# Kernel tuning notes

Hardware: AMD Instinct MI355X
Metric: run time of the kernel (lower is better)

Reference implementation:

```python
import jax, jax.numpy as jnp
import numpy as np
from math import sqrt

NUM_ENT = 100000
NUM_REL = 237  # base; rel table has 2*NUM_REL rows
DIM = 200
HALF = DIM // 2


def _lrelu(x, slope):
    return jnp.where(x >= 0, x, slope * x)


def setup_inputs() -> dict:
    key = jax.random.key(0)
    ks = jax.random.split(key, 20)
    s = 0.02
    inp = {
        'edge_index': jax.random.randint(ks[0], (2, 500000), 0, NUM_ENT),
        'edge_type': jax.random.randint(ks[1], (500000,), 0, 2 * NUM_REL),
        'toTest': jax.random.randint(ks[2], (131072, 2), 0, NUM_ENT),
        'ent_emb': s * jax.random.normal(ks[3], (NUM_ENT, DIM), jnp.float32),
        'rel_emb': s * jax.random.normal(ks[4], (2 * NUM_REL, DIM), jnp.float32),
        'W': s * jax.random.normal(ks[5], (DIM, DIM), jnp.float32),
        'W_loop': s * jax.random.normal(ks[6], (DIM, DIM), jnp.float32),
        'W_rel': s * jax.random.normal(ks[7], (DIM, DIM), jnp.float32),
        'trans_w': s * jax.random.normal(ks[8], (DIM, HALF), jnp.float32),
        'trans_b': jnp.zeros((HALF,), jnp.float32),
        'q_w': s * jax.random.normal(ks[9], (HALF, 128), jnp.float32),
        'q_b': jnp.zeros((128,), jnp.float32),
        'k_w': s * jax.random.normal(ks[10], (HALF, 128), jnp.float32),
        'k_b': jnp.zeros((128,), jnp.float32),
        'w1': s * jax.random.normal(ks[11], (DIM * 2 + 1 + 2 * NUM_REL, 2048), jnp.float32),
        'b1': jnp.zeros((2048,), jnp.float32),
        'w2': s * jax.random.normal(ks[12], (2048, 512), jnp.float32),
        'b2': jnp.zeros((512,), jnp.float32),
        'w3': s * jax.random.normal(ks[13], (512, 1), jnp.float32),
        'b3': jnp.zeros((1,), jnp.float32),
    }
    return inp


def reference(ent_emb, rel_emb, W, W_loop, W_rel, trans_w, trans_b,
              q_w, q_b, k_w, k_b, w1, b1, w2, b2, w3, b3,
              edge_index, edge_type, toTest):
    # --- CompGCN base layer ('sub' composition, degree-normalized scatter-add) ---
    src, dst = edge_index[0], edge_index[1]
    msg = (ent_emb[src] - rel_emb[edge_type]) @ W          # [E, D] gather + GEMM
    deg = jax.ops.segment_sum(jnp.ones_like(dst, jnp.float32), dst, num_segments=NUM_ENT)
    norm = jax.lax.rsqrt(jnp.maximum(deg, 1.0))
    agg = jax.ops.segment_sum(msg, dst, num_segments=NUM_ENT) * norm[:, None]
    all_ent = jnp.tanh(agg + ent_emb @ W_loop)             # [num_ent, D]
    all_rel = rel_emb @ W_rel                              # [2*num_rel, D]

    # --- PairRE test scoring path ---
    head_rel = all_rel[:, :HALF]                           # [2R, D/2]
    tail_rel = all_rel[:, HALF:]
    te = all_ent[toTest]                                   # [N, 2, D] gather
    ee = te @ trans_w + trans_b                            # [N, 2, D/2]
    h_e, t_e = ee[:, 0], ee[:, 1]
    atta = ((h_e @ q_w + q_b) * (t_e @ k_w + k_b)).sum(-1, keepdims=True) / sqrt(DIM)
    relSim = h_e @ head_rel.T - t_e @ tail_rel.T           # [N, 2R]
    cat = jnp.concatenate([te[:, 0], te[:, 1], atta, relSim], axis=1)
    h1 = _lrelu(cat @ w1 + b1, 1e-4)
    h2 = _lrelu(h1 @ w2 + b2, 1e-3)
    return jax.nn.sigmoid(h2 @ w3 + b3)                    # [N, 1]
```

## Files before the change

kernel.cpp:

```cpp
#include <hip/hip_runtime.h>

typedef unsigned short u16;
typedef unsigned long long u64;
typedef __attribute__((ext_vector_type(8))) short bf8;
typedef __attribute__((ext_vector_type(4))) float fx4;

#define N_ENT   100000
#define N_EDGE  500000
#define N_TEST  131072
#define EDIM    200
#define AE_LD   224
#define NB_SCAN 391

__device__ __forceinline__ u16 f2bf(float f) {
  union { float f; unsigned u; } c; c.f = f;
  return (u16)((c.u + 0x7FFFu + ((c.u >> 16) & 1u)) >> 16);
}
__device__ __forceinline__ float bf2f(u16 h) {
  union { unsigned u; float f; } c; c.u = ((unsigned)h) << 16;
  return c.f;
}
__device__ __forceinline__ void gload16(const u16* g, u16* l) {
  __builtin_amdgcn_global_load_lds(
      (const __attribute__((address_space(1))) void*)g,
      (__attribute__((address_space(3))) void*)l, 16, 0, 0);
}

#define BK 32
#define EPS 72

template<int TM, int WN>
__global__ __launch_bounds__(64 * 2 * WN) void gemm_t(
    const u16* __restrict__ A, long lda,
    const u16* __restrict__ B, long ldb,
    u16* __restrict__ out, long ldOut,
    int K, int NBN,
    const int* __restrict__ rowIdx, int idxMode, int mClamp,
    int mValid, int nValid, int nStore,
    const float* __restrict__ bias, int act, float slope,
    const u16* __restrict__ qbuf, const float* __restrict__ auxF,
    float* __restrict__ dotOut)
{
  constexpr int BM = TM * 32;
  constexpr int BN = WN * 64;
  constexpr int BUFS = (BM + BN) * BK;
  __shared__ __align__(16) u16 smem[2 * BUFS];
  const int tid  = threadIdx.x;
  const int wave = tid >> 6, lane = tid & 63;
  const int wr = (wave / WN) * (TM * 16), wc = (wave % WN) * 64;
  const int fr = lane & 15, fq = lane >> 4;

  const int nwg = gridDim.x;
  const int orig = blockIdx.x;
  const int q = nwg >> 3, rr = nwg & 7;
  const int xcd = orig & 7, j = orig >> 3;
  const int wgid = (xcd < rr ? xcd * (q + 1) : rr * (q + 1) + (xcd - rr) * q) + j;
  const long bm = (long)(wgid / NBN) * BM;
  const long bn = (long)(wgid % NBN) * BN;

  const int srow = wave * 32;
  const int kc = (((lane & 3) ^ ((lane >> 3) & 3)) * 8);
  long a0[2], a1[2], boff[2];
  #pragma unroll
  for (int h = 0; h < 2; ++h) {
    long gmRow = bm + srow + h * 16 + (lane >> 2);
    long b0, b1;
    if (idxMode == 0) {
      long gm = (gmRow >= mClamp) ? (mClamp - 1) : gmRow;
      b0 = gm * lda; b1 = b0;
    } else if (idxMode == 2) {
      b0 = (long)rowIdx[2 * gmRow] * lda; b1 = b0;
    } else if (idxMode == 3) {
      b0 = (long)rowIdx[2 * gmRow + 1] * lda; b1 = b0;
    } else {
      b0 = (long)rowIdx[2 * gmRow] * lda;
      b1 = (long)rowIdx[2 * gmRow + 1] * lda - 224;
    }
    a0[h] = b0 + kc; a1[h] = b1 + kc;
    boff[h] = (bn + srow + h * 16 + (lane >> 2)) * ldb + kc;
  }

  auto STAGE = [&](int buf, int k0) {
    u16* Ad = smem + buf * BUFS;
    u16* Bd = Ad + BM * BK;
    const bool lo = (k0 + kc) < 224;
    #pragma unroll
    for (int h = 0; h < 2; ++h) {
      const long ao = (idxMode == 4) ? (lo ? a0[h] : a1[h]) : a0[h];
      gload16(A + ao + k0, &Ad[(srow + h * 16) * BK]);
      gload16(B + boff[h] + k0, &Bd[(srow + h * 16) * BK]);
    }
  };

  fx4 zero4 = {0.f, 0.f, 0.f, 0.f};
  fx4 acc[TM][4];
  #pragma unroll
  for (int i = 0; i < TM; ++i)
    #pragma unroll
    for (int j2 = 0; j2 < 4; ++j2) acc[i][j2] = zero4;

  const int NT = K / BK;
  STAGE(0, 0);
  for (int t = 0; t < NT; ++t) {
    const int cur = t & 1;
    if (t + 1 < NT) {
      STAGE(cur ^ 1, (t + 1) * BK);
      __builtin_amdgcn_sched_barrier(0);
      asm volatile("s_waitcnt vmcnt(4)" ::: "memory");
    } else {
      __builtin_amdgcn_sched_barrier(0);
      asm volatile("s_waitcnt vmcnt(0)" ::: "memory");
    }
    __builtin_amdgcn_sched_barrier(0);
    __builtin_amdgcn_s_barrier();
    __builtin_amdgcn_sched_barrier(0);
    {
      const u16* Ac = smem + cur * BUFS;
      const u16* Bc = Ac + BM * BK;
      bf8 aF[TM], bF[4];
      const int rslot = (fq ^ ((fr >> 1) & 3)) * 8;
      #pragma unroll
      for (int mt = 0; mt < TM; ++mt)
        aF[mt] = *(const bf8*)&Ac[(wr + mt * 16 + fr) * BK + rslot];
      #pragma unroll
      for (int nt = 0; nt < 4; ++nt)
        bF[nt] = *(const bf8*)&Bc[(wc + nt * 16 + fr) * BK + rslot];
      #pragma unroll
      for (int mt = 0; mt < TM; ++mt)
        #pragma unroll
        for (int nt = 0; nt < 4; ++nt)
          acc[mt][nt] = __builtin_amdgcn_mfma_f32_16x16x32_bf16(aF[mt], bF[nt], acc[mt][nt], 0, 0, 0);
    }
    __builtin_amdgcn_sched_barrier(0);
    __builtin_amdgcn_s_barrier();
    __builtin_amdgcn_sched_barrier(0);
  }

  if (act == 3 || act == 4) {
    #pragma unroll
    for (int mt = 0; mt < TM; ++mt) {
      #pragma unroll
      for (int r = 0; r < 4; ++r) {
        const long gm = bm + wr + mt * 16 + fq * 4 + r;
        float p = 0.f;
        #pragma unroll
        for (int nt = 0; nt < 4; ++nt) {
          const long gn = bn + wc + nt * 16 + fr;
          float v = acc[mt][nt][r] + bias[gn];
          if (act == 3) p += v * bf2f(qbuf[gm * 128 + gn]);
          else { v = (v >= 0.f) ? v : v * slope; p += v * auxF[gn]; }
        }
        p += __shfl_xor(p, 1, 64); p += __shfl_xor(p, 2, 64);
        p += __shfl_xor(p, 4, 64); p += __shfl_xor(p, 8, 64);
        if (fr == 0 && gm < mValid)
          atomicAdd(&dotOut[gm], (act == 3) ? p * 0.07071067811865475f : p);
      }
    }
    return;
  }

  u16* ep = smem + wave * (32 * EPS);
  #pragma unroll
  for (int p = 0; p < TM / 2; ++p) {
    #pragma unroll
    for (int mt2 = 0; mt2 < 2; ++mt2) {
      const int mt = 2 * p + mt2;
      #pragma unroll
      for (int r = 0; r < 4; ++r) {
        const int lrl = mt2 * 16 + fq * 4 + r;
        const long gm = bm + wr + mt * 16 + fq * 4 + r;
        const float attaV = (act == 5) ? dotOut[gm] : 0.f;
        #pragma unroll
        for (int nt = 0; nt < 4; ++nt) {
          const long gn = bn + wc + nt * 16 + fr;
          float v = 0.f;
          if (gn < nValid) {
            v = acc[mt][nt][r];
            if (bias) v += bias[gn];
            if (act == 1) v = tanhf(v);
            else if (act == 5) { v += attaV * auxF[gn]; v = (v >= 0.f) ? v : v * slope; }
          }
          ep[lrl * EPS + nt * 16 + fr] = f2bf(v);
        }
      }
    }
    #pragma unroll
    for (int it = 0; it < 4; ++it) {
      const int lr = it * 8 + (lane >> 3);
      const int lc = (lane & 7) * 8;
      const long gm = bm + wr + p * 32 + lr;
      const long gn = bn + wc + lc;
      if (gm < mValid && gn + 7 < nStore)
        *(bf8*)(out + gm * ldOut + gn) = *(const bf8*)&ep[lr * EPS + lc];
    }
  }
}

__global__ void hist_kernel(const int* __restrict__ ei, int* __restrict__ cnt) {
  int e = blockIdx.x * 256 + threadIdx.x;
  if (e < N_EDGE) atomicAdd(&cnt[ei[N_EDGE + e]], 1);
}
__global__ void scanA_kernel(const int* __restrict__ cnt, int* __restrict__ offs,
                             int* __restrict__ blockSums) {
  __shared__ int s[256];
  int gid = blockIdx.x * 256 + threadIdx.x;
  int v = (gid < N_ENT) ? cnt[gid] : 0;
  s[threadIdx.x] = v;
  __syncthreads();
  for (int off = 1; off < 256; off <<= 1) {
    int t = (threadIdx.x >= off) ? s[threadIdx.x - off] : 0;
    __syncthreads();
    s[threadIdx.x] += t;
    __syncthreads();
  }
  if (gid < N_ENT) offs[gid] = s[threadIdx.x] - v;
  if (threadIdx.x == 255) blockSums[blockIdx.x] = s[255];
}
__global__ void scanB_kernel(const int* __restrict__ blockSums, int* __restrict__ blockOffs) {
  __shared__ int s[512];
  int v = (threadIdx.x < NB_SCAN) ? blockSums[threadIdx.x] : 0;
  s[threadIdx.x] = v;
  __syncthreads();
  for (int off = 1; off < 512; off <<= 1) {
    int t = (threadIdx.x >= off) ? s[threadIdx.x - off] : 0;
    __syncthreads();
    s[threadIdx.x] += t;
    __syncthreads();
  }
  if (threadIdx.x < NB_SCAN) blockOffs[threadIdx.x] = s[threadIdx.x] - v;
}
__global__ void scanC_kernel(int* __restrict__ offs, const int* __restrict__ blockOffs) {
  int gid = blockIdx.x * 256 + threadIdx.x;
  if (gid < N_ENT) offs[gid] += blockOffs[blockIdx.x];
}
__global__ void place_kernel(const int* __restrict__ ei, const int* __restrict__ et,
                             const int* __restrict__ offs, int* __restrict__ cursor,
                             int* __restrict__ sortedSrc, int* __restrict__ sortedT) {
  int e = blockIdx.x * 256 + threadIdx.x;
  if (e >= N_EDGE) return;
  int dst = ei[N_EDGE + e];
  int pos = offs[dst] + atomicAdd(&cursor[dst], 1);
  sortedSrc[pos] = ei[e];
  sortedT[pos]   = et[e];
}
__global__ void agg_A1_kernel(const int* __restrict__ offs, const int* __restrict__ cnt,
                              const int* __restrict__ sortedSrc, const int* __restrict__ sortedT,
                              const float* __restrict__ ent_emb, const float* __restrict__ rel_emb,
                              u16* __restrict__ A1) {
  const int r = blockIdx.x * 4 + (threadIdx.x >> 6);
  if (r >= N_ENT) return;
  const int lane = threadIdx.x & 63;
  const int beg = offs[r], n = cnt[r];
  u16* row = A1 + (size_t)r * 416;
  if (lane < 50) {
    float4 a = {0.f, 0.f, 0.f, 0.f};
    for (int e = 0; e < n; ++e) {
      const int s = sortedSrc[beg + e], t = sortedT[beg + e];
      float4 x = ((const float4*)(ent_emb + (size_t)s * EDIM))[lane];
      float4 y = ((const float4*)(rel_emb + (size_t)t * EDIM))[lane];
      a.x += x.x - y.x; a.y += x.y - y.y; a.z += x.z - y.z; a.w += x.w - y.w;
    }
    const float nm = rsqrtf(fmaxf((float)n, 1.f));
    u64 p = (u64)f2bf(a.x * nm) | ((u64)f2bf(a.y * nm) << 16)
          | ((u64)f2bf(a.z * nm) << 32) | ((u64)f2bf(a.w * nm) << 48);
    *(u64*)(row + 4 * lane) = p;
    float4 e = ((const float4*)(ent_emb + (size_t)r * EDIM))[lane];
    u64 q = (u64)f2bf(e.x) | ((u64)f2bf(e.y) << 16)
          | ((u64)f2bf(e.z) << 32) | ((u64)f2bf(e.w) << 48);
    *(u64*)(row + 200 + 4 * lane) = q;
  }
  if (lane < 16) row[400 + lane] = 0;
}

__global__ void build_B1T(const float* __restrict__ W, const float* __restrict__ W_loop,
                          u16* __restrict__ B1T)
{
  int idx = blockIdx.x * 256 + threadIdx.x;
  if (idx >= 256 * 416) return;
  int n = idx / 416, k = idx % 416;
  float v = 0.f;
  if (n < 200) {
    if (k < 200) v = W[k * 200 + n];
    else if (k < 400) v = W_loop[(k - 200) * 200 + n];
  }
  B1T[idx] = f2bf(v);
}
__global__ void all_rel_kernel(const float* __restrict__ rel_emb, const float* __restrict__ W_rel,
                               float* __restrict__ all_rel)
{
  int r = blockIdx.x, c = threadIdx.x;
  if (c >= 200) return;
  const float* re = rel_emb + r * 200;
  float a = 0.f;
  for (int k = 0; k < 200; ++k) a += re[k] * W_rel[k * 200 + c];
  all_rel[r * 200 + c] = a;
}
__global__ void pq_kernel(const float* __restrict__ all_rel, const float* __restrict__ w1,
                          float* __restrict__ PQ) {
  int idx = blockIdx.x * 256 + threadIdx.x;
  if (idx >= 2 * 100 * 2048) return;
  int n = idx & 2047, m = (idx >> 11) % 100, sel = idx / 204800;
  float a = 0.f;
  for (int r = 0; r < 474; ++r)
    a += all_rel[r * 200 + sel * 100 + m] * w1[(size_t)(401 + r) * 2048 + n];
  PQ[idx] = a;
}
__global__ void p2_kernel(const float* __restrict__ trans_w, const float* __restrict__ PQ,
                          float* __restrict__ P2) {
  int idx = blockIdx.x * 256 + threadIdx.x;
  if (idx >= 2 * 200 * 2048) return;
  int n = idx & 2047, k = (idx >> 11) % 200, sel = idx / 409600;
  const float* pq = PQ + sel * 204800;
  float a = 0.f;
  for (int m = 0; m < 100; ++m) a += trans_w[k * 100 + m] * pq[m * 2048 + n];
  P2[idx] = a;
}
__global__ void w1eff_kernel(const float* __restrict__ w1, const float* __restrict__ P2,
                             u16* __restrict__ W1eff) {
  int idx = blockIdx.x * 256 + threadIdx.x;
  if (idx >= 2048 * 448) return;
  int n = idx / 448, k = idx % 448;
  float v = 0.f;
  if (k < 200) v = w1[(size_t)k * 2048 + n] + P2[(size_t)k * 2048 + n];
  else if (k >= 224 && k < 424) {
    int kk = k - 224;
    v = w1[(size_t)(200 + kk) * 2048 + n] - P2[409600 + (size_t)kk * 2048 + n];
  }
  W1eff[idx] = f2bf(v);
}
__global__ void b1eff_kernel(const float* __restrict__ b1, const float* __restrict__ trans_b,
                             const float* __restrict__ PQ, float* __restrict__ b1eff) {
  int n = blockIdx.x * 256 + threadIdx.x;
  if (n >= 2048) return;
  float a = b1[n];
  for (int m = 0; m < 100; ++m)
    a += trans_b[m] * (PQ[m * 2048 + n] - PQ[204800 + m * 2048 + n]);
  b1eff[n] = a;
}
__global__ void qkw2_kernel(const float* __restrict__ trans_w, const float* __restrict__ q_w,
                            const float* __restrict__ k_w, u16* __restrict__ qw2T,
                            u16* __restrict__ kw2T) {
  int idx = blockIdx.x * 256 + threadIdx.x;
  if (idx >= 128 * 224) return;
  int j = idx / 224, k = idx % 224;
  float a = 0.f, b = 0.f;
  if (k < 200)
    for (int m = 0; m < 100; ++m) {
      float t = trans_w[k * 100 + m];
      a += t * q_w[m * 128 + j];
      b += t * k_w[m * 128 + j];
    }
  qw2T[idx] = f2bf(a);
  kw2T[idx] = f2bf(b);
}
__global__ void qkb2_kernel(const float* __restrict__ q_b, const float* __restrict__ k_b,
                            const float* __restrict__ trans_b, const float* __restrict__ q_w,
                            const float* __restrict__ k_w, float* __restrict__ qb2,
                            float* __restrict__ kb2) {
  int j = threadIdx.x;
  if (j >= 128) return;
  float a = q_b[j], b = k_b[j];
  for (int m = 0; m < 100; ++m) {
    a += trans_b[m] * q_w[m * 128 + j];
    b += trans_b[m] * k_w[m * 128 + j];
  }
  qb2[j] = a; kb2[j] = b;
}
__global__ void build_w2T(const float* __restrict__ w2, u16* __restrict__ w2T)
{
  long idx = (long)blockIdx.x * 256 + threadIdx.x;
  if (idx >= (long)512 * 2048) return;
  int n = (int)(idx / 2048), k = (int)(idx % 2048);
  w2T[idx] = f2bf(w2[(size_t)k * 512 + n]);
}
__global__ void sigmoid_kernel(const float* __restrict__ logit, const float* __restrict__ b3,
                               float* __restrict__ out) {
  int i = blockIdx.x * 256 + threadIdx.x;
  if (i >= N_TEST) return;
  out[i] = 1.f / (1.f + __expf(-(logit[i] + b3[0])));
}

extern "C" void kernel_launch(void* const* d_in, const int* in_sizes, int n_in,
                              void* d_out, int out_size, void* d_ws, size_t ws_size,
                              hipStream_t stream)
{
  (void)in_sizes; (void)n_in; (void)out_size;
  const int*   edge_index = (const int*)d_in[0];
  const int*   edge_type  = (const int*)d_in[1];
  const int*   toTest     = (const int*)d_in[2];
  const float* ent_emb    = (const float*)d_in[3];
  const float* rel_emb    = (const float*)d_in[4];
  const float* W          = (const float*)d_in[5];
  const float* W_loop     = (const float*)d_in[6];
  const float* W_rel      = (const float*)d_in[7];
  const float* trans_w    = (const float*)d_in[8];
  const float* trans_b    = (const float*)d_in[9];
  const float* q_w        = (const float*)d_in[10];
  const float* q_b        = (const float*)d_in[11];
  const float* k_w        = (const float*)d_in[12];
  const float* k_b        = (const float*)d_in[13];
  const float* w1         = (const float*)d_in[14];
  const float* b1         = (const float*)d_in[15];
  const float* w2         = (const float*)d_in[16];
  const float* b2         = (const float*)d_in[17];
  const float* w3         = (const float*)d_in[18];
  const float* b3         = (const float*)d_in[19];
  float* out = (float*)d_out;

  unsigned char* ws = (unsigned char*)d_ws;
  float* atta    = (float*)(ws + 0);
  float* logit   = (float*)(ws + 524288);
  float* allrel  = (float*)(ws + 1048576);
  u16*   B1T     = (u16*)  (ws + 1427968);
  u16*   W1eff   = (u16*)  (ws + 1640960);
  u16*   qw2T    = (u16*)  (ws + 3475968);
  u16*   kw2T    = (u16*)  (ws + 3533312);
  float* b1eff   = (float*)(ws + 3590656);
  float* qb2     = (float*)(ws + 3598848);
  float* kb2     = (float*)(ws + 3599872);
  u16*   w2T     = (u16*)  (ws + 3600896);
  const size_t X_base = 5698048;
  u16*   all_ent = (u16*)  (ws + X_base);
  u16*   Qbuf    = (u16*)  (ws + X_base + 44800000);
  const size_t Y_base = 84052480;
  u16*   A1      = (u16*)  (ws + Y_base);
  const size_t Z_base = 167252480;

  int*   cnt       = (int*)  (ws + Z_base);
  int*   offs      = (int*)  (ws + Z_base + 400000);
  int*   cursor    = (int*)  (ws + Z_base + 800000);
  int*   blockSums = (int*)  (ws + Z_base + 1200000);
  int*   blockOffs = (int*)  (ws + Z_base + 1202048);
  int*   sortedSrc = (int*)  (ws + Z_base + 1204096);
  int*   sortedT   = (int*)  (ws + Z_base + 3204096);
  float* PQ        = (float*)(ws + Z_base + 5204096);
  float* P2        = (float*)(ws + Z_base + 6842496);

  int CH;
  if      (Z_base + (size_t)131072 * 4096 <= ws_size) CH = 131072;
  else if (Z_base + (size_t)65536  * 4096 <= ws_size) CH = 65536;
  else if (Z_base + (size_t)32768  * 4096 <= ws_size) CH = 32768;
  else if (Z_base + (size_t)16384  * 4096 <= ws_size) CH = 16384;
  else if (Z_base + (size_t)8192   * 4096 <= ws_size) CH = 8192;
  else return;
  u16* h1 = (u16*)(ws + Z_base);
  const int NC = N_TEST / CH;

  hipMemsetAsync(cnt, 0, 400000, stream);
  hipMemsetAsync(cursor, 0, 400000, stream);
  hipMemsetAsync(atta, 0, 524288, stream);
  hipMemsetAsync(logit, 0, 524288, stream);

  hist_kernel<<<(N_EDGE + 255) / 256, 256, 0, stream>>>(edge_index, cnt);
  scanA_kernel<<<NB_SCAN, 256, 0, stream>>>(cnt, offs, blockSums);
  scanB_kernel<<<1, 512, 0, stream>>>(blockSums, blockOffs);
  scanC_kernel<<<NB_SCAN, 256, 0, stream>>>(offs, blockOffs);
  place_kernel<<<(N_EDGE + 255) / 256, 256, 0, stream>>>(edge_index, edge_type, offs, cursor,
                                                         sortedSrc, sortedT);
  agg_A1_kernel<<<(N_ENT + 3) / 4, 256, 0, stream>>>(offs, cnt, sortedSrc, sortedT,
                                                     ent_emb, rel_emb, A1);
  build_B1T<<<(256 * 416) / 256, 256, 0, stream>>>(W, W_loop, B1T);

  gemm_t<4, 2><<<782 * 2, 256, 0, stream>>>(A1, 416, B1T, 416, all_ent, AE_LD,
      416, 2, nullptr, 0, N_ENT, N_ENT, 200, AE_LD, nullptr, 1, 0.f,
      nullptr, nullptr, nullptr);

  all_rel_kernel<<<474, 256, 0, stream>>>(rel_emb, W_rel, allrel);
  pq_kernel<<<(2 * 100 * 2048) / 256, 256, 0, stream>>>(allrel, w1, PQ);
  p2_kernel<<<(2 * 200 * 2048) / 256, 256, 0, stream>>>(trans_w, PQ, P2);
  w1eff_kernel<<<(2048 * 448) / 256, 256, 0, stream>>>(w1, P2, W1eff);
  b1eff_kernel<<<8, 256, 0, stream>>>(b1, trans_b, PQ, b1eff);
  qkw2_kernel<<<(128 * 224) / 256, 256, 0, stream>>>(trans_w, q_w, k_w, qw2T, kw2T);
  qkb2_kernel<<<1, 128, 0, stream>>>(q_b, k_b, trans_b, q_w, k_w, qb2, kb2);
  build_w2T<<<(512 * 2048) / 256, 256, 0, stream>>>(w2, w2T);

  gemm_t<4, 2><<<1024, 256, 0, stream>>>(all_ent, AE_LD, qw2T, AE_LD, Qbuf, 128,
      AE_LD, 1, toTest, 2, 0, N_TEST, 128, 128, qb2, 0, 0.f,
      nullptr, nullptr, nullptr);
  gemm_t<4, 2><<<1024, 256, 0, stream>>>(all_ent, AE_LD, kw2T, AE_LD, nullptr, 0,
      AE_LD, 1, toTest, 3, 0, N_TEST, 128, 128, kb2, 3, 0.f,
      Qbuf, nullptr, atta);

  for (int c = 0; c < NC; ++c) {
    gemm_t<4, 2><<<(CH / 128) * 16, 256, 0, stream>>>(all_ent, AE_LD, W1eff, 448, h1, 2048,
        448, 16, toTest + (size_t)c * CH * 2, 4, 0, CH, 2048, 2048, b1eff, 5, 0.0001f,
        nullptr, w1 + (size_t)400 * 2048, atta + (size_t)c * CH);
    gemm_t<4, 2><<<(CH / 128) * 4, 256, 0, stream>>>(h1, 2048, w2T, 2048, nullptr, 0,
        2048, 4, nullptr, 0, CH, CH, 512, 512, b2, 4, 0.001f,
        nullptr, w3, logit + (size_t)c * CH);
  }
  sigmoid_kernel<<<N_TEST / 256, 256, 0, stream>>>(logit, b3, out);
}
```

Measured before the change: 1.666 ms.

## Add triple-buffered pipelined GEMM path with larger tiles for MLP layers

```diff
diff --git a/kernel.cpp b/kernel.cpp
--- a/kernel.cpp
+++ b/kernel.cpp
@@ -29,7 +29,7 @@
 #define BK 32
 #define EPS 72
 
-template<int TM, int WN>
+template<int TM, int WN, int PIPE>
 __global__ __launch_bounds__(64 * 2 * WN) void gemm_t(
     const u16* __restrict__ A, long lda,
     const u16* __restrict__ B, long ldb,
@@ -44,7 +44,8 @@
   constexpr int BM = TM * 32;
   constexpr int BN = WN * 64;
   constexpr int BUFS = (BM + BN) * BK;
-  __shared__ __align__(16) u16 smem[2 * BUFS];
+  constexpr int NBUF = PIPE ? 3 : 2;
+  __shared__ __align__(16) u16 smem[NBUF * BUFS];
   const int tid  = threadIdx.x;
   const int wave = tid >> 6, lane = tid & 63;
   const int wr = (wave / WN) * (TM * 16), wc = (wave % WN) * 64;
@@ -100,40 +101,97 @@
     for (int j2 = 0; j2 < 4; ++j2) acc[i][j2] = zero4;
 
   const int NT = K / BK;
-  STAGE(0, 0);
-  for (int t = 0; t < NT; ++t) {
-    const int cur = t & 1;
-    if (t + 1 < NT) {
-      STAGE(cur ^ 1, (t + 1) * BK);
-      __builtin_amdgcn_sched_barrier(0);
-      asm volatile("s_waitcnt vmcnt(4)" ::: "memory");
-    } else {
-      __builtin_amdgcn_sched_barrier(0);
-      asm volatile("s_waitcnt vmcnt(0)" ::: "memory");
-    }
+  const int rslot = (fq ^ ((fr >> 1) & 3)) * 8;
+
+  if constexpr (PIPE == 0) {
+    STAGE(0, 0);
+    for (int t = 0; t < NT; ++t) {
+      const int cur = t & 1;
+      if (t + 1 < NT) {
+        STAGE(cur ^ 1, (t + 1) * BK);
+        __builtin_amdgcn_sched_barrier(0);
+        asm volatile("s_waitcnt vmcnt(4)" ::: "memory");
+      } else {
+        __builtin_amdgcn_sched_barrier(0);
+        asm volatile("s_waitcnt vmcnt(0)" ::: "memory");
+      }
+      __builtin_amdgcn_sched_barrier(0);
+      __builtin_amdgcn_s_barrier();
+      __builtin_amdgcn_sched_barrier(0);
+      {
+        const u16* Ac = smem + cur * BUFS;
+        const u16* Bc = Ac + BM * BK;
+        bf8 aF[TM], bF[4];
+        #pragma unroll
+        for (int mt = 0; mt < TM; ++mt)
+          aF[mt] = *(const bf8*)&Ac[(wr + mt * 16 + fr) * BK + rslot];
+        #pragma unroll
+        for (int nt = 0; nt < 4; ++nt)
+          bF[nt] = *(const bf8*)&Bc[(wc + nt * 16 + fr) * BK + rslot];
+        #pragma unroll
+        for (int mt = 0; mt < TM; ++mt)
+          #pragma unroll
+          for (int nt = 0; nt < 4; ++nt)
+            acc[mt][nt] = __builtin_amdgcn_mfma_f32_16x16x32_bf16(aF[mt], bF[nt], acc[mt][nt], 0, 0, 0);
+      }
+      __builtin_amdgcn_sched_barrier(0);
+      __builtin_amdgcn_s_barrier();
+      __builtin_amdgcn_sched_barrier(0);
+    }
+  } else {
+    constexpr int HM = TM / 2;
+    STAGE(0, 0);
+    if (NT > 1) STAGE(1, BK);
+    __builtin_amdgcn_sched_barrier(0);
+    if (NT > 1) asm volatile("s_waitcnt vmcnt(4)" ::: "memory");
+    else        asm volatile("s_waitcnt vmcnt(0)" ::: "memory");
     __builtin_amdgcn_sched_barrier(0);
     __builtin_amdgcn_s_barrier();
     __builtin_amdgcn_sched_barrier(0);
-    {
-      const u16* Ac = smem + cur * BUFS;
+    for (int t = 0; t < NT; ++t) {
+      const u16* Ac = smem + (t % 3) * BUFS;
       const u16* Bc = Ac + BM * BK;
-      bf8 aF[TM], bF[4];
-      const int rslot = (fq ^ ((fr >> 1) & 3)) * 8;
-      #pragma unroll
-      for (int mt = 0; mt < TM; ++mt)
-        aF[mt] = *(const bf8*)&Ac[(wr + mt * 16 + fr) * BK + rslot];
-      #pragma unroll
-      for (int nt = 0; nt < 4; ++nt)
-        bF[nt] = *(const bf8*)&Bc[(wc + nt * 16 + fr) * BK + rslot];
-      #pragma unroll
-      for (int mt = 0; mt < TM; ++mt)
+      if (t + 2 < NT) STAGE((t + 2) % 3, (t + 2) * BK);
+      __builtin_amdgcn_sched_barrier(0);
+      bf8 bF[4], aF[HM];
+      #pragma unroll
+      for (int x = 0; x < 4; ++x)
+        bF[x] = *(const bf8*)&Bc[(wc + x * 16 + fr) * BK + rslot];
+      #pragma unroll
+      for (int x = 0; x < HM; ++x)
+        aF[x] = *(const bf8*)&Ac[(wr + x * 16 + fr) * BK + rslot];
+      asm volatile("s_waitcnt lgkmcnt(0)" ::: "memory");
+      __builtin_amdgcn_sched_barrier(0);
+      __builtin_amdgcn_s_setprio(1);
+      #pragma unroll
+      for (int mt = 0; mt < HM; ++mt)
         #pragma unroll
         for (int nt = 0; nt < 4; ++nt)
           acc[mt][nt] = __builtin_amdgcn_mfma_f32_16x16x32_bf16(aF[mt], bF[nt], acc[mt][nt], 0, 0, 0);
-    }
-    __builtin_amdgcn_sched_barrier(0);
-    __builtin_amdgcn_s_barrier();
-    __builtin_amdgcn_sched_barrier(0);
+      __builtin_amdgcn_s_setprio(0);
+      __builtin_amdgcn_sched_barrier(0);
+      __builtin_amdgcn_s_barrier();
+      __builtin_amdgcn_sched_barrier(0);
+      bf8 aG[HM];
+      #pragma unroll
+      for (int x = 0; x < HM; ++x)
+        aG[x] = *(const bf8*)&Ac[(wr + (x + HM) * 16 + fr) * BK + rslot];
+      asm volatile("s_waitcnt lgkmcnt(0)" ::: "memory");
+      __builtin_amdgcn_sched_barrier(0);
+      __builtin_amdgcn_s_setprio(1);
+      #pragma unroll
+      for (int mt = 0; mt < HM; ++mt)
+        #pragma unroll
+        for (int nt = 0; nt < 4; ++nt)
+          acc[mt + HM][nt] = __builtin_amdgcn_mfma_f32_16x16x32_bf16(aG[mt], bF[nt], acc[mt + HM][nt], 0, 0, 0);
+      __builtin_amdgcn_s_setprio(0);
+      __builtin_amdgcn_sched_barrier(0);
+      if (t + 2 < NT) asm volatile("s_waitcnt vmcnt(4)" ::: "memory");
+      else            asm volatile("s_waitcnt vmcnt(0)" ::: "memory");
+      __builtin_amdgcn_sched_barrier(0);
+      __builtin_amdgcn_s_barrier();
+      __builtin_amdgcn_sched_barrier(0);
+    }
   }
 
   if (act == 3 || act == 4) {
@@ -461,7 +519,7 @@
                                                      ent_emb, rel_emb, A1);
   build_B1T<<<(256 * 416) / 256, 256, 0, stream>>>(W, W_loop, B1T);
 
-  gemm_t<4, 2><<<782 * 2, 256, 0, stream>>>(A1, 416, B1T, 416, all_ent, AE_LD,
+  gemm_t<4, 2, 0><<<782 * 2, 256, 0, stream>>>(A1, 416, B1T, 416, all_ent, AE_LD,
       416, 2, nullptr, 0, N_ENT, N_ENT, 200, AE_LD, nullptr, 1, 0.f,
       nullptr, nullptr, nullptr);
 
@@ -474,19 +532,19 @@
   qkb2_kernel<<<1, 128, 0, stream>>>(q_b, k_b, trans_b, q_w, k_w, qb2, kb2);
   build_w2T<<<(512 * 2048) / 256, 256, 0, stream>>>(w2, w2T);
 
-  gemm_t<4, 2><<<1024, 256, 0, stream>>>(all_ent, AE_LD, qw2T, AE_LD, Qbuf, 128,
+  gemm_t<4, 2, 0><<<1024, 256, 0, stream>>>(all_ent, AE_LD, qw2T, AE_LD, Qbuf, 128,
       AE_LD, 1, toTest, 2, 0, N_TEST, 128, 128, qb2, 0, 0.f,
       nullptr, nullptr, nullptr);
-  gemm_t<4, 2><<<1024, 256, 0, stream>>>(all_ent, AE_LD, kw2T, AE_LD, nullptr, 0,
+  gemm_t<4, 2, 0><<<1024, 256, 0, stream>>>(all_ent, AE_LD, kw2T, AE_LD, nullptr, 0,
       AE_LD, 1, toTest, 3, 0, N_TEST, 128, 128, kb2, 3, 0.f,
       Qbuf, nullptr, atta);
 
   for (int c = 0; c < NC; ++c) {
-    gemm_t<4, 2><<<(CH / 128) * 16, 256, 0, stream>>>(all_ent, AE_LD, W1eff, 448, h1, 2048,
-        448, 16, toTest + (size_t)c * CH * 2, 4, 0, CH, 2048, 2048, b1eff, 5, 0.0001f,
+    gemm_t<8, 4, 1><<<(CH / 256) * 8, 512, 0, stream>>>(all_ent, AE_LD, W1eff, 448, h1, 2048,
+        448, 8, toTest + (size_t)c * CH * 2, 4, 0, CH, 2048, 2048, b1eff, 5, 0.0001f,
         nullptr, w1 + (size_t)400 * 2048, atta + (size_t)c * CH);
-    gemm_t<4, 2><<<(CH / 128) * 4, 256, 0, stream>>>(h1, 2048, w2T, 2048, nullptr, 0,
-        2048, 4, nullptr, 0, CH, CH, 512, 512, b2, 4, 0.001f,
+    gemm_t<8, 4, 1><<<(CH / 256) * 2, 512, 0, stream>>>(h1, 2048, w2T, 2048, nullptr, 0,
+        2048, 2, nullptr, 0, CH, CH, 512, 512, b2, 4, 0.001f,
         nullptr, w3, logit + (size_t)c * CH);
   }
   sigmoid_kernel<<<N_TEST / 256, 256, 0, stream>>>(logit, b3, out);
```

New measurement: 1.677 ms. No clear change (+0.6%).
